# Performance work log

Hardware: AMD Instinct MI355X
Metric: run time of the kernel (lower is better)

The kernel has to match this reference:

```python
import jax, jax.numpy as jnp
import numpy as np

L, B, S, D, H, F, V = 12, 2, 1024, 768, 12, 3072, 50257
DK = D // H
EPS = 1e-6


def _ln(x, a, b):
    # torch: a*(x-mean)/(std+eps)+b with unbiased std (ddof=1)
    m = x.mean(-1, keepdims=True)
    std = jnp.sqrt(((x - m) ** 2).sum(-1, keepdims=True) / (x.shape[-1] - 1))
    return a * (x - m) / (std + EPS) + b


def _pos_encoding(s, d):
    pos = jnp.arange(s, dtype=jnp.float32)[:, None]
    div = jnp.exp(jnp.arange(0, d, 2, dtype=jnp.float32) * (-np.log(10000.0) / d))
    pe = jnp.zeros((s, d), dtype=jnp.float32)
    pe = pe.at[:, 0::2].set(jnp.sin(pos * div))
    pe = pe.at[:, 1::2].set(jnp.cos(pos * div))
    return pe


def setup_inputs() -> dict:
    key = jax.random.key(0)
    ks = jax.random.split(key, 8)
    n = lambda k, sh: 0.02 * jax.random.normal(k, sh, dtype=jnp.float32)
    return dict(
        emb=n(ks[0], (V, D)),
        Wq=n(ks[1], (L, D, D)),
        Wk=n(ks[2], (L, D, D)),
        Wv=n(ks[3], (L, D, D)),
        Wo=n(ks[4], (L, D, D)),
        ln1_a=jnp.ones((L, D), jnp.float32),
        ln1_b=jnp.zeros((L, D), jnp.float32),
        ln2_a=jnp.ones((L, D), jnp.float32),
        ln2_b=jnp.zeros((L, D), jnp.float32),
        W1=n(ks[5], (L, D, F)),
        b1=jnp.zeros((L, F), jnp.float32),
        W2=n(ks[6], (L, F, D)),
        b2=jnp.zeros((L, D), jnp.float32),
        fn_a=jnp.ones((D,), jnp.float32),
        fn_b=jnp.zeros((D,), jnp.float32),
        pb=jnp.zeros((V,), jnp.float32),
        x=jax.random.randint(ks[7], (B, S), 0, V, dtype=jnp.int32),
    )


def reference(emb, Wq, Wk, Wv, Wo, ln1_a, ln1_b, ln2_a, ln2_b, W1, b1, W2, b2, fn_a, fn_b, pb, x):
    b, s = x.shape
    d = emb.shape[1]
    h = emb[x] * jnp.sqrt(jnp.float32(d)) + _pos_encoding(s, d)  # [B,S,D]
    causal = jnp.tril(jnp.ones((s, s), dtype=bool))

    def block(hh, p):
        wq, wk, wv, wo, a1, bb1n, a2, bb2n, w1, fb1, w2, fb2 = p
        xn = _ln(hh, a1, bb1n)
        q = (xn @ wq).reshape(b, s, H, DK)
        k = (xn @ wk).reshape(b, s, H, DK)
        v = (xn @ wv).reshape(b, s, H, DK)
        scores = jnp.einsum('bqhd,bkhd->bhqk', q, k) / jnp.sqrt(jnp.float32(DK))
        scores = jnp.where(causal, scores, -1e9)  # masked_fill_(mask==0, -1e9)
        attn = jax.nn.softmax(scores, axis=-1)
        o = jnp.einsum('bhqk,bkhd->bqhd', attn, v).reshape(b, s, d)
        hh = hh + o @ wo
        xn2 = _ln(hh, a2, bb2n)
        hh = hh + (jax.nn.relu(xn2 @ w1 + fb1) @ w2 + fb2)
        return hh, None

    h, _ = jax.lax.scan(block, h, (Wq, Wk, Wv, Wo, ln1_a, ln1_b, ln2_a, ln2_b, W1, b1, W2, b2))
    h = _ln(h, fn_a, fn_b)
    logits = h @ emb.T + pb  # tied-weight projection
    return logits
```

## Files before the change

### kernel.cpp

```cpp
#include <hip/hip_runtime.h>
#include <math.h>

constexpr int Lc = 12, Bc = 2, Sc = 1024, Dc = 768, Hc = 12, Fc = 3072, Vc = 50257, DKc = 64;
constexpr int Tc = Bc * Sc;
constexpr int QKVN = 3 * Dc;
constexpr int Vpad = 50304;

typedef __attribute__((ext_vector_type(8))) __bf16 bf16x8;
typedef __attribute__((ext_vector_type(8))) unsigned short u16x8;
typedef __attribute__((ext_vector_type(4))) float f32x4;

__device__ __forceinline__ unsigned short f2b(float f) {
  union { float f; unsigned int u; } v; v.f = f;
  unsigned int r = v.u + 0x7FFFu + ((v.u >> 16) & 1u);
  return (unsigned short)(r >> 16);
}
__device__ __forceinline__ float b2f(unsigned short u) {
  return __uint_as_float(((unsigned int)u) << 16);
}

__device__ __forceinline__ void gload16(const void* g, void* l) {
  __builtin_amdgcn_global_load_lds((const __attribute__((address_space(1))) void*)g,
                                   (__attribute__((address_space(3))) void*)l, 16, 0, 0);
}

__device__ __forceinline__ float bred_sum(float v, volatile float* sb) {
#pragma unroll
  for (int o = 32; o; o >>= 1) v += __shfl_down(v, o);
  int w = threadIdx.x >> 6;
  __syncthreads();
  if ((threadIdx.x & 63) == 0) sb[w] = v;
  __syncthreads();
  return sb[0] + sb[1] + sb[2] + sb[3];
}

__global__ __launch_bounds__(256) void embed_kernel(const float* __restrict__ emb,
                                                    const int* __restrict__ x,
                                                    float* __restrict__ h) {
  int t = blockIdx.x;
  int s = t & (Sc - 1);
  int tok = x[t];
  const float scale = 27.712812921102035f;
  for (int d = threadIdx.x; d < Dc; d += 256) {
    int i = d >> 1;
    float div = __expf((float)(2 * i) * (-9.210340371976184f / (float)Dc));
    float ang = (float)s * div;
    float pe = (d & 1) ? cosf(ang) : sinf(ang);
    h[(size_t)t * Dc + d] = emb[(size_t)tok * Dc + d] * scale + pe;
  }
}

__global__ __launch_bounds__(256) void convert_emb_kernel(const float* __restrict__ emb,
                                                          ushort* __restrict__ embT) {
  const size_t total4 = (size_t)Vpad * Dc / 4;
  for (size_t i = (size_t)blockIdx.x * 256 + threadIdx.x; i < total4; i += (size_t)gridDim.x * 256) {
    size_t e = i * 4;
    int row = (int)(e / Dc);
    ushort4 w;
    if (row < Vc) {
      float4 f = *(const float4*)&emb[e];
      w.x = f2b(f.x); w.y = f2b(f.y); w.z = f2b(f.z); w.w = f2b(f.w);
    } else {
      w = make_ushort4(0, 0, 0, 0);
    }
    *(ushort4*)&embT[e] = w;
  }
}

__global__ __launch_bounds__(256) void transpose_layer_kernel(
    const float* __restrict__ Wq, const float* __restrict__ Wk, const float* __restrict__ Wv,
    const float* __restrict__ Wo, const float* __restrict__ W1, const float* __restrict__ W2,
    int l, ushort* __restrict__ WqkvT, ushort* __restrict__ WoT,
    ushort* __restrict__ W1T, ushort* __restrict__ W2T) {
  __shared__ float tile[64][65];
  int bid = blockIdx.x;
  const float* src; ushort* dst; int N, Kd, tt;
  if (bid < 432) {
    int m = bid / 144; tt = bid % 144;
    src = (m == 0 ? Wq : (m == 1 ? Wk : Wv)) + (size_t)l * Dc * Dc;
    N = Dc; Kd = Dc; dst = WqkvT + (size_t)m * Dc * Dc;
  } else if (bid < 576) {
    tt = bid - 432; src = Wo + (size_t)l * Dc * Dc; N = Dc; Kd = Dc; dst = WoT;
  } else if (bid < 1152) {
    tt = bid - 576; src = W1 + (size_t)l * Dc * Fc; N = Fc; Kd = Dc; dst = W1T;
  } else {
    tt = bid - 1152; src = W2 + (size_t)l * Fc * Dc; N = Dc; Kd = Fc; dst = W2T;
  }
  int nt = N / 64;
  int k0 = (tt / nt) * 64, n0 = (tt % nt) * 64;
  int t = threadIdx.x;
  int r0 = t >> 4, c4 = (t & 15) * 4;
#pragma unroll
  for (int rr = 0; rr < 4; ++rr) {
    int r = r0 + rr * 16;
    float4 f = *(const float4*)&src[(size_t)(k0 + r) * N + n0 + c4];
    tile[r][c4] = f.x; tile[r][c4 + 1] = f.y; tile[r][c4 + 2] = f.z; tile[r][c4 + 3] = f.w;
  }
  __syncthreads();
  int i0 = t >> 4, j4 = (t & 15) * 4;
#pragma unroll
  for (int rr = 0; rr < 4; ++rr) {
    int i = i0 + rr * 16;
    ushort4 w;
    w.x = f2b(tile[j4][i]); w.y = f2b(tile[j4 + 1][i]);
    w.z = f2b(tile[j4 + 2][i]); w.w = f2b(tile[j4 + 3][i]);
    *(ushort4*)&dst[(size_t)(n0 + i) * Kd + k0 + j4] = w;
  }
}

__global__ __launch_bounds__(256) void ln_kernel(const float* __restrict__ in,
                                                 const float* __restrict__ ga,
                                                 const float* __restrict__ be,
                                                 ushort* __restrict__ out) {
  __shared__ float sb[4];
  int t = blockIdx.x;
  const float* row = in + (size_t)t * Dc;
  int tid = threadIdx.x;
  float x0 = row[tid], x1 = row[tid + 256], x2 = row[tid + 512];
  float s = bred_sum(x0 + x1 + x2, sb);
  float mean = s * (1.0f / 768.0f);
  float d0 = x0 - mean, d1 = x1 - mean, d2 = x2 - mean;
  float vs = bred_sum(d0 * d0 + d1 * d1 + d2 * d2, sb);
  float inv = 1.0f / (sqrtf(vs * (1.0f / 767.0f)) + 1e-6f);
  ushort* orow = out + (size_t)t * Dc;
  orow[tid] = f2b(ga[tid] * d0 * inv + be[tid]);
  orow[tid + 256] = f2b(ga[tid + 256] * d1 * inv + be[tid + 256]);
  orow[tid + 512] = f2b(ga[tid + 512] * d2 * inv + be[tid + 512]);
}

template <typename OT, int BM, bool BIAS, bool RELU, bool RESID, bool SWAP>
__global__ __launch_bounds__(256) void gemm_bf16(const ushort* __restrict__ A,
                                                 const ushort* __restrict__ Bt,
                                                 const float* __restrict__ bias,
                                                 const float* __restrict__ resid,
                                                 OT* __restrict__ C,
                                                 int M, int N, int K, int ldc) {
  constexpr int MW = BM / 64;
  constexpr int NW = 4 / MW;
  constexpr int WCOLS = 128 / NW;
  constexpr int NJ = WCOLS / 16;
  __shared__ __attribute__((aligned(16))) ushort sm[(BM + 128) * 32];
  ushort* As = sm;
  ushort* Bs = sm + BM * 32;
  const int tid = threadIdx.x;
  const int wid = tid >> 6, lane = tid & 63;
  const int wr = (MW == 2) ? (wid >> 1) : 0;
  const int wc = (MW == 2) ? (wid & 1) : wid;
  const int kg = lane >> 4, fr = lane & 15;
  const int bm = (SWAP ? blockIdx.x : blockIdx.y) * BM;
  const int bn = (SWAP ? blockIdx.y : blockIdx.x) * 128;

  f32x4 acc[4][NJ] = {};

  for (int k0 = 0; k0 < K; k0 += 32) {
    const ushort* Ab = A + (size_t)bm * K + k0;
    const ushort* Bb = Bt + (size_t)bn * K + k0;
#pragma unroll
    for (int it = 0; it < BM / 64; ++it) {
      int c = it * 256 + tid;
      int row = c >> 2, kc = (c & 3) * 8;
      gload16(Ab + (size_t)row * K + kc, &As[(it * 256 + wid * 64) * 8]);
    }
#pragma unroll
    for (int it = 0; it < 2; ++it) {
      int c = it * 256 + tid;
      int row = c >> 2, kc = (c & 3) * 8;
      gload16(Bb + (size_t)row * K + kc, &Bs[(it * 256 + wid * 64) * 8]);
    }
    __syncthreads();

    bf16x8 af[4], bfr[NJ];
#pragma unroll
    for (int i = 0; i < 4; ++i)
      af[i] = *(const bf16x8*)&As[(wr * 64 + i * 16 + fr) * 32 + kg * 8];
#pragma unroll
    for (int j = 0; j < NJ; ++j)
      bfr[j] = *(const bf16x8*)&Bs[(wc * WCOLS + j * 16 + fr) * 32 + kg * 8];
#pragma unroll
    for (int i = 0; i < 4; ++i)
#pragma unroll
      for (int j = 0; j < NJ; ++j)
        acc[i][j] = __builtin_amdgcn_mfma_f32_16x16x32_bf16(af[i], bfr[j], acc[i][j], 0, 0, 0);
    __syncthreads();
  }

  const int r0 = kg * 4;
#pragma unroll
  for (int i = 0; i < 4; ++i) {
    int mbase = bm + wr * 64 + i * 16 + r0;
#pragma unroll
    for (int j = 0; j < NJ; ++j) {
      int n = bn + wc * WCOLS + j * 16 + fr;
      if (n < N) {
        float bv = BIAS ? bias[n] : 0.0f;
#pragma unroll
        for (int r = 0; r < 4; ++r) {
          float v = acc[i][j][r] + bv;
          if (RELU) v = fmaxf(v, 0.0f);
          size_t idx = (size_t)(mbase + r) * ldc + n;
          if (RESID) v += resid[idx];
          if constexpr (sizeof(OT) == 2) C[idx] = (OT)f2b(v);
          else C[idx] = (OT)v;
        }
      }
    }
  }
}

__global__ __launch_bounds__(256) void flash_attn_kernel(const ushort* __restrict__ qkv,
                                                         ushort* __restrict__ o) {
  const int qt = gridDim.x - 1 - blockIdx.x;
  const int hb = blockIdx.y;
  const int hh = hb % Hc, b = hb / Hc;
  const int tid = threadIdx.x;
  const int w = tid >> 6, lane = tid & 63;
  const int g = lane >> 4, c = lane & 15;

  __shared__ __attribute__((aligned(16))) ushort Ks[64 * 64];
  __shared__ __attribute__((aligned(16))) ushort Vt[64 * 64];
  __shared__ __attribute__((aligned(16))) ushort Ps[4][16 * 64];

  const int q0 = qt * 64;
  const int qw = q0 + w * 16;

  bf16x8 aq[2];
  {
    const size_t qrow = (size_t)(b * Sc + qw + c) * QKVN + hh * DKc;
#pragma unroll
    for (int kk = 0; kk < 2; ++kk)
      aq[kk] = *(const bf16x8*)&qkv[qrow + kk * 32 + g * 8];
  }

  float m_r[4], l_r[4];
  f32x4 oa[4] = {};
#pragma unroll
  for (int r = 0; r < 4; ++r) { m_r[r] = -1e30f; l_r[r] = 0.f; }

  const int ntiles = qt + 1;
  for (int t = 0; t < ntiles; ++t) {
    const int kv0 = t * 64;
#pragma unroll
    for (int it = 0; it < 2; ++it) {
      int idx = it * 256 + tid;
      int kv = idx >> 3, ck = idx & 7;
      u16x8 kd = *(const u16x8*)&qkv[(size_t)(b * Sc + kv0 + kv) * QKVN + Dc + hh * DKc + ck * 8];
      *(u16x8*)((char*)Ks + ((kv * 128 + ck * 16) ^ ((kv & 7) << 4))) = kd;
    }
    {
      int kv = tid >> 2;
      int dbase = (tid & 3) * 16;
      const ushort* vrow = &qkv[(size_t)(b * Sc + kv0 + kv) * QKVN + 2 * Dc + hh * DKc + dbase];
      u16x8 v0 = *(const u16x8*)&vrow[0];
      u16x8 v1 = *(const u16x8*)&vrow[8];
#pragma unroll
      for (int dd = 0; dd < 8; ++dd) {
        int d0 = dbase + dd, d1 = dbase + 8 + dd;
        *(ushort*)((char*)Vt + ((d0 * 128 + kv * 2) ^ ((d0 & 7) << 4))) = v0[dd];
        *(ushort*)((char*)Vt + ((d1 * 128 + kv * 2) ^ ((d1 & 7) << 4))) = v1[dd];
      }
    }
    __syncthreads();

    f32x4 sacc[4] = {};
#pragma unroll
    for (int jn = 0; jn < 4; ++jn) {
      int kvl = jn * 16 + c;
#pragma unroll
      for (int kk = 0; kk < 2; ++kk) {
        bf16x8 bk = *(const bf16x8*)((char*)Ks + ((kvl * 128 + kk * 64 + g * 16) ^ ((kvl & 7) << 4)));
        sacc[jn] = __builtin_amdgcn_mfma_f32_16x16x32_bf16(aq[kk], bk, sacc[jn], 0, 0, 0);
      }
    }

    const bool last = (t == ntiles - 1);
    float p[4][4];
#pragma unroll
    for (int jn = 0; jn < 4; ++jn) {
      int kvg = kv0 + jn * 16 + c;
#pragma unroll
      for (int r = 0; r < 4; ++r) {
        float s = sacc[jn][r] * 0.125f;
        if (last && kvg > qw + g * 4 + r) s = -1e30f;
        p[jn][r] = s;
      }
    }
#pragma unroll
    for (int r = 0; r < 4; ++r) {
      float mx = fmaxf(fmaxf(p[0][r], p[1][r]), fmaxf(p[2][r], p[3][r]));
#pragma unroll
      for (int off = 1; off < 16; off <<= 1) mx = fmaxf(mx, __shfl_xor(mx, off));
      float mnew = fmaxf(m_r[r], mx);
      float sf = __expf(m_r[r] - mnew);
      m_r[r] = mnew;
      float rs = 0.f;
#pragma unroll
      for (int jn = 0; jn < 4; ++jn) {
        float e = __expf(p[jn][r] - mnew);
        p[jn][r] = e;
        rs += e;
      }
#pragma unroll
      for (int off = 1; off < 16; off <<= 1) rs += __shfl_xor(rs, off);
      l_r[r] = l_r[r] * sf + rs;
#pragma unroll
      for (int jd = 0; jd < 4; ++jd) oa[jd][r] *= sf;
    }

    {
      ushort* pw = Ps[w];
#pragma unroll
      for (int jn = 0; jn < 4; ++jn)
#pragma unroll
        for (int r = 0; r < 4; ++r) {
          int row = g * 4 + r, col = jn * 16 + c;
          *(ushort*)((char*)pw + ((row * 128 + col * 2) ^ ((row & 7) << 4))) = f2b(p[jn][r]);
        }
      bf16x8 ap[2];
#pragma unroll
      for (int kk = 0; kk < 2; ++kk)
        ap[kk] = *(const bf16x8*)((char*)pw + ((c * 128 + kk * 64 + g * 16) ^ ((c & 7) << 4)));
#pragma unroll
      for (int jd = 0; jd < 4; ++jd) {
        int d = jd * 16 + c;
#pragma unroll
        for (int kk = 0; kk < 2; ++kk) {
          bf16x8 bv = *(const bf16x8*)((char*)Vt + ((d * 128 + kk * 64 + g * 16) ^ ((d & 7) << 4)));
          oa[jd] = __builtin_amdgcn_mfma_f32_16x16x32_bf16(ap[kk], bv, oa[jd], 0, 0, 0);
        }
      }
    }
    __syncthreads();
  }

#pragma unroll
  for (int r = 0; r < 4; ++r) {
    int q = qw + g * 4 + r;
    float inv = 1.0f / l_r[r];
    size_t base = (size_t)(b * Sc + q) * Dc + hh * DKc;
#pragma unroll
    for (int jd = 0; jd < 4; ++jd)
      o[base + jd * 16 + c] = f2b(oa[jd][r] * inv);
  }
}

extern "C" void kernel_launch(void* const* d_in, const int* in_sizes, int n_in,
                              void* d_out, int out_size, void* d_ws, size_t ws_size,
                              hipStream_t stream) {
  const float* emb  = (const float*)d_in[0];
  const float* Wq   = (const float*)d_in[1];
  const float* Wk   = (const float*)d_in[2];
  const float* Wv   = (const float*)d_in[3];
  const float* Wo   = (const float*)d_in[4];
  const float* ln1a = (const float*)d_in[5];
  const float* ln1b = (const float*)d_in[6];
  const float* ln2a = (const float*)d_in[7];
  const float* ln2b = (const float*)d_in[8];
  const float* W1   = (const float*)d_in[9];
  const float* b1   = (const float*)d_in[10];
  const float* W2   = (const float*)d_in[11];
  const float* b2   = (const float*)d_in[12];
  const float* fna  = (const float*)d_in[13];
  const float* fnb  = (const float*)d_in[14];
  const float* pb   = (const float*)d_in[15];
  const int*   x    = (const int*)d_in[16];
  float* out = (float*)d_out;

  float* h = (float*)d_ws;
  ushort* xn    = (ushort*)(h + (size_t)Tc * Dc);
  ushort* qkv   = xn + (size_t)Tc * Dc;
  ushort* ao    = qkv + (size_t)Tc * QKVN;
  ushort* f1    = ao + (size_t)Tc * Dc;
  ushort* embT  = f1 + (size_t)Tc * Fc;
  ushort* WqkvT = embT + (size_t)Vpad * Dc;
  ushort* WoT   = WqkvT + (size_t)QKVN * Dc;
  ushort* W1T   = WoT + (size_t)Dc * Dc;
  ushort* W2T   = W1T + (size_t)Fc * Dc;

  embed_kernel<<<Tc, 256, 0, stream>>>(emb, x, h);
  convert_emb_kernel<<<2048, 256, 0, stream>>>(emb, embT);

  dim3 gQKV(QKVN / 128, Tc / 128);
  dim3 gD64(Dc / 128, Tc / 64);
  dim3 gF(Fc / 128, Tc / 128);
  dim3 gA(Sc / 64, Bc * Hc);
  for (int l = 0; l < Lc; ++l) {
    transpose_layer_kernel<<<1728, 256, 0, stream>>>(Wq, Wk, Wv, Wo, W1, W2, l,
                                                     WqkvT, WoT, W1T, W2T);
    ln_kernel<<<Tc, 256, 0, stream>>>(h, ln1a + l * Dc, ln1b + l * Dc, xn);
    gemm_bf16<ushort, 128, false, false, false, false><<<gQKV, 256, 0, stream>>>(
        xn, WqkvT, nullptr, nullptr, qkv, Tc, QKVN, Dc, QKVN);
    flash_attn_kernel<<<gA, 256, 0, stream>>>(qkv, ao);
    gemm_bf16<float, 64, false, false, true, false><<<gD64, 256, 0, stream>>>(
        ao, WoT, nullptr, h, h, Tc, Dc, Dc, Dc);
    ln_kernel<<<Tc, 256, 0, stream>>>(h, ln2a + l * Dc, ln2b + l * Dc, xn);
    gemm_bf16<ushort, 128, true, true, false, false><<<gF, 256, 0, stream>>>(
        xn, W1T, b1 + (size_t)l * Fc, nullptr, f1, Tc, Fc, Dc, Fc);
    gemm_bf16<float, 64, true, false, true, false><<<gD64, 256, 0, stream>>>(
        f1, W2T, b2 + (size_t)l * Dc, h, h, Tc, Dc, Fc, Dc);
  }
  ln_kernel<<<Tc, 256, 0, stream>>>(h, fna, fnb, xn);
  dim3 gL(Tc / 128, Vpad / 128);
  gemm_bf16<float, 128, true, false, false, true><<<gL, 256, 0, stream>>>(
      xn, embT, pb, nullptr, out, Tc, Vc, Dc, Vc);
}
```

Baseline: 3.010 ms.

## Deepen GEMM K-tile, add V pre-transpose, widen attention KV tiles

The GEMM K-step doubles from 32 to 64, so there are half as many barrier-separated iterations and more MFMA work per LDS fill. A separate kernel writes V transposed per head, which lets the attention kernel load K and V straight into swizzled LDS with global_load_lds instead of scattered scalar stores. Attention now handles 128 KV positions per tile and uses exp2 with a log2e-folded scale. In exchange there is one extra kernel launch and round trip through memory per layer, more LDS per block (which may lower occupancy), and partial masking on the last tile when the query tile index is even.

```diff
diff --git a/kernel.cpp b/kernel.cpp
--- a/kernel.cpp
+++ b/kernel.cpp
@@ -108,6 +108,31 @@
   }
 }
 
+__global__ __launch_bounds__(256) void vtrans_kernel(const ushort* __restrict__ qkv,
+                                                     ushort* __restrict__ vT) {
+  __shared__ ushort tl[64][72];
+  const int st = blockIdx.x, hb = blockIdx.y;
+  const int hh = hb % Hc, b = hb / Hc;
+  const int t0 = st * 64;
+  const int tid = threadIdx.x;
+  {
+    int r = tid >> 2, cg = (tid & 3) * 16;
+    const ushort* src = qkv + (size_t)(b * Sc + t0 + r) * QKVN + 2 * Dc + hh * DKc + cg;
+    *(u16x8*)&tl[r][cg] = *(const u16x8*)&src[0];
+    *(u16x8*)&tl[r][cg + 8] = *(const u16x8*)&src[8];
+  }
+  __syncthreads();
+  {
+    int d = tid >> 2, tg = (tid & 3) * 16;
+    u16x8 o0, o1;
+#pragma unroll
+    for (int j = 0; j < 8; ++j) { o0[j] = tl[tg + j][d]; o1[j] = tl[tg + 8 + j][d]; }
+    ushort* dst = vT + (size_t)hb * DKc * Sc + (size_t)d * Sc + t0 + tg;
+    *(u16x8*)&dst[0] = o0;
+    *(u16x8*)&dst[8] = o1;
+  }
+}
+
 __global__ __launch_bounds__(256) void ln_kernel(const float* __restrict__ in,
                                                  const float* __restrict__ ga,
                                                  const float* __restrict__ be,
@@ -139,9 +164,9 @@
   constexpr int NW = 4 / MW;
   constexpr int WCOLS = 128 / NW;
   constexpr int NJ = WCOLS / 16;
-  __shared__ __attribute__((aligned(16))) ushort sm[(BM + 128) * 32];
+  __shared__ __attribute__((aligned(16))) ushort sm[(BM + 128) * 64];
   ushort* As = sm;
-  ushort* Bs = sm + BM * 32;
+  ushort* Bs = sm + BM * 64;
   const int tid = threadIdx.x;
   const int wid = tid >> 6, lane = tid & 63;
   const int wr = (MW == 2) ? (wid >> 1) : 0;
@@ -152,35 +177,38 @@
 
   f32x4 acc[4][NJ] = {};
 
-  for (int k0 = 0; k0 < K; k0 += 32) {
+  for (int k0 = 0; k0 < K; k0 += 64) {
     const ushort* Ab = A + (size_t)bm * K + k0;
     const ushort* Bb = Bt + (size_t)bn * K + k0;
 #pragma unroll
-    for (int it = 0; it < BM / 64; ++it) {
-      int c = it * 256 + tid;
-      int row = c >> 2, kc = (c & 3) * 8;
+    for (int it = 0; it < BM / 32; ++it) {
+      int s = it * 256 + tid;
+      int row = s >> 3, kc = (s & 7) * 8;
       gload16(Ab + (size_t)row * K + kc, &As[(it * 256 + wid * 64) * 8]);
     }
 #pragma unroll
-    for (int it = 0; it < 2; ++it) {
-      int c = it * 256 + tid;
-      int row = c >> 2, kc = (c & 3) * 8;
+    for (int it = 0; it < 4; ++it) {
+      int s = it * 256 + tid;
+      int row = s >> 3, kc = (s & 7) * 8;
       gload16(Bb + (size_t)row * K + kc, &Bs[(it * 256 + wid * 64) * 8]);
     }
     __syncthreads();
 
-    bf16x8 af[4], bfr[NJ];
-#pragma unroll
-    for (int i = 0; i < 4; ++i)
-      af[i] = *(const bf16x8*)&As[(wr * 64 + i * 16 + fr) * 32 + kg * 8];
-#pragma unroll
-    for (int j = 0; j < NJ; ++j)
-      bfr[j] = *(const bf16x8*)&Bs[(wc * WCOLS + j * 16 + fr) * 32 + kg * 8];
-#pragma unroll
-    for (int i = 0; i < 4; ++i)
+#pragma unroll
+    for (int hk = 0; hk < 2; ++hk) {
+      bf16x8 af[4], bfr[NJ];
+#pragma unroll
+      for (int i = 0; i < 4; ++i)
+        af[i] = *(const bf16x8*)&As[(wr * 64 + i * 16 + fr) * 64 + hk * 32 + kg * 8];
 #pragma unroll
       for (int j = 0; j < NJ; ++j)
-        acc[i][j] = __builtin_amdgcn_mfma_f32_16x16x32_bf16(af[i], bfr[j], acc[i][j], 0, 0, 0);
+        bfr[j] = *(const bf16x8*)&Bs[(wc * WCOLS + j * 16 + fr) * 64 + hk * 32 + kg * 8];
+#pragma unroll
+      for (int i = 0; i < 4; ++i)
+#pragma unroll
+        for (int j = 0; j < NJ; ++j)
+          acc[i][j] = __builtin_amdgcn_mfma_f32_16x16x32_bf16(af[i], bfr[j], acc[i][j], 0, 0, 0);
+    }
     __syncthreads();
   }
 
@@ -208,6 +236,7 @@
 }
 
 __global__ __launch_bounds__(256) void flash_attn_kernel(const ushort* __restrict__ qkv,
+                                                         const ushort* __restrict__ vT,
                                                          ushort* __restrict__ o) {
   const int qt = gridDim.x - 1 - blockIdx.x;
   const int hb = blockIdx.y;
@@ -216,9 +245,9 @@
   const int w = tid >> 6, lane = tid & 63;
   const int g = lane >> 4, c = lane & 15;
 
-  __shared__ __attribute__((aligned(16))) ushort Ks[64 * 64];
-  __shared__ __attribute__((aligned(16))) ushort Vt[64 * 64];
-  __shared__ __attribute__((aligned(16))) ushort Ps[4][16 * 64];
+  __shared__ __attribute__((aligned(16))) ushort Ks[128 * 64];
+  __shared__ __attribute__((aligned(16))) ushort Vs[64 * 128];
+  __shared__ __attribute__((aligned(16))) ushort Ps[4][16 * 128];
 
   const int q0 = qt * 64;
   const int qw = q0 + w * 16;
@@ -236,34 +265,34 @@
 #pragma unroll
   for (int r = 0; r < 4; ++r) { m_r[r] = -1e30f; l_r[r] = 0.f; }
 
-  const int ntiles = qt + 1;
-  for (int t = 0; t < ntiles; ++t) {
-    const int kv0 = t * 64;
-#pragma unroll
-    for (int it = 0; it < 2; ++it) {
-      int idx = it * 256 + tid;
-      int kv = idx >> 3, ck = idx & 7;
-      u16x8 kd = *(const u16x8*)&qkv[(size_t)(b * Sc + kv0 + kv) * QKVN + Dc + hh * DKc + ck * 8];
-      *(u16x8*)((char*)Ks + ((kv * 128 + ck * 16) ^ ((kv & 7) << 4))) = kd;
-    }
-    {
-      int kv = tid >> 2;
-      int dbase = (tid & 3) * 16;
-      const ushort* vrow = &qkv[(size_t)(b * Sc + kv0 + kv) * QKVN + 2 * Dc + hh * DKc + dbase];
-      u16x8 v0 = *(const u16x8*)&vrow[0];
-      u16x8 v1 = *(const u16x8*)&vrow[8];
-#pragma unroll
-      for (int dd = 0; dd < 8; ++dd) {
-        int d0 = dbase + dd, d1 = dbase + 8 + dd;
-        *(ushort*)((char*)Vt + ((d0 * 128 + kv * 2) ^ ((d0 & 7) << 4))) = v0[dd];
-        *(ushort*)((char*)Vt + ((d1 * 128 + kv * 2) ^ ((d1 & 7) << 4))) = v1[dd];
-      }
+  const ushort* kbase = qkv + (size_t)b * Sc * QKVN + Dc + hh * DKc;
+  const ushort* vbase = vT + (size_t)hb * DKc * Sc;
+  const float kS = 0.18033688011112042f;
+
+  const int KT = (qt + 2) >> 1;
+  for (int t = 0; t < KT; ++t) {
+    const int kv0 = t * 128;
+#pragma unroll
+    for (int it = 0; it < 4; ++it) {
+      int s = it * 256 + tid;
+      int kv = s >> 3;
+      int dkb = ((s & 7) * 16) ^ ((kv & 7) << 4);
+      gload16(kbase + (size_t)(kv0 + kv) * QKVN + (dkb >> 1),
+              (char*)Ks + (it * 256 + w * 64) * 16);
+    }
+#pragma unroll
+    for (int it = 0; it < 4; ++it) {
+      int s = it * 256 + tid;
+      int d = s >> 4;
+      int kvb = ((s & 15) * 16) ^ ((d & 7) << 4);
+      gload16(vbase + (size_t)d * Sc + kv0 + (kvb >> 1),
+              (char*)Vs + (it * 256 + w * 64) * 16);
     }
     __syncthreads();
 
-    f32x4 sacc[4] = {};
-#pragma unroll
-    for (int jn = 0; jn < 4; ++jn) {
+    f32x4 sacc[8] = {};
+#pragma unroll
+    for (int jn = 0; jn < 8; ++jn) {
       int kvl = jn * 16 + c;
 #pragma unroll
       for (int kk = 0; kk < 2; ++kk) {
@@ -272,31 +301,35 @@
       }
     }
 
-    const bool last = (t == ntiles - 1);
-    float p[4][4];
-#pragma unroll
-    for (int jn = 0; jn < 4; ++jn) {
-      int kvg = kv0 + jn * 16 + c;
-#pragma unroll
-      for (int r = 0; r < 4; ++r) {
-        float s = sacc[jn][r] * 0.125f;
-        if (last && kvg > qw + g * 4 + r) s = -1e30f;
-        p[jn][r] = s;
+#pragma unroll
+    for (int jn = 0; jn < 8; ++jn)
+#pragma unroll
+      for (int r = 0; r < 4; ++r) sacc[jn][r] *= kS;
+    if (t == KT - 1) {
+#pragma unroll
+      for (int jn = 0; jn < 8; ++jn) {
+        int kvg = kv0 + jn * 16 + c;
+#pragma unroll
+        for (int r = 0; r < 4; ++r)
+          if (kvg > qw + g * 4 + r) sacc[jn][r] = -1e30f;
       }
     }
+
 #pragma unroll
     for (int r = 0; r < 4; ++r) {
-      float mx = fmaxf(fmaxf(p[0][r], p[1][r]), fmaxf(p[2][r], p[3][r]));
+      float mx = sacc[0][r];
+#pragma unroll
+      for (int jn = 1; jn < 8; ++jn) mx = fmaxf(mx, sacc[jn][r]);
 #pragma unroll
       for (int off = 1; off < 16; off <<= 1) mx = fmaxf(mx, __shfl_xor(mx, off));
       float mnew = fmaxf(m_r[r], mx);
-      float sf = __expf(m_r[r] - mnew);
+      float sf = exp2f(m_r[r] - mnew);
       m_r[r] = mnew;
       float rs = 0.f;
 #pragma unroll
-      for (int jn = 0; jn < 4; ++jn) {
-        float e = __expf(p[jn][r] - mnew);
-        p[jn][r] = e;
+      for (int jn = 0; jn < 8; ++jn) {
+        float e = exp2f(sacc[jn][r] - mnew);
+        sacc[jn][r] = e;
         rs += e;
       }
 #pragma unroll
@@ -309,22 +342,22 @@
     {
       ushort* pw = Ps[w];
 #pragma unroll
-      for (int jn = 0; jn < 4; ++jn)
+      for (int jn = 0; jn < 8; ++jn)
 #pragma unroll
         for (int r = 0; r < 4; ++r) {
           int row = g * 4 + r, col = jn * 16 + c;
-          *(ushort*)((char*)pw + ((row * 128 + col * 2) ^ ((row & 7) << 4))) = f2b(p[jn][r]);
+          *(ushort*)((char*)pw + ((row * 256 + col * 2) ^ ((row & 7) << 4))) = f2b(sacc[jn][r]);
         }
-      bf16x8 ap[2];
-#pragma unroll
-      for (int kk = 0; kk < 2; ++kk)
-        ap[kk] = *(const bf16x8*)((char*)pw + ((c * 128 + kk * 64 + g * 16) ^ ((c & 7) << 4)));
+      bf16x8 ap[4];
+#pragma unroll
+      for (int kk = 0; kk < 4; ++kk)
+        ap[kk] = *(const bf16x8*)((char*)pw + ((c * 256 + kk * 64 + g * 16) ^ ((c & 7) << 4)));
 #pragma unroll
       for (int jd = 0; jd < 4; ++jd) {
         int d = jd * 16 + c;
 #pragma unroll
-        for (int kk = 0; kk < 2; ++kk) {
-          bf16x8 bv = *(const bf16x8*)((char*)Vt + ((d * 128 + kk * 64 + g * 16) ^ ((d & 7) << 4)));
+        for (int kk = 0; kk < 4; ++kk) {
+          bf16x8 bv = *(const bf16x8*)((char*)Vs + ((d * 256 + kk * 64 + g * 16) ^ ((d & 7) << 4)));
           oa[jd] = __builtin_amdgcn_mfma_f32_16x16x32_bf16(ap[kk], bv, oa[jd], 0, 0, 0);
         }
       }
@@ -370,7 +403,8 @@
   ushort* qkv   = xn + (size_t)Tc * Dc;
   ushort* ao    = qkv + (size_t)Tc * QKVN;
   ushort* f1    = ao + (size_t)Tc * Dc;
-  ushort* embT  = f1 + (size_t)Tc * Fc;
+  ushort* vT    = f1 + (size_t)Tc * Fc;
+  ushort* embT  = vT + (size_t)Bc * Hc * DKc * Sc;
   ushort* WqkvT = embT + (size_t)Vpad * Dc;
   ushort* WoT   = WqkvT + (size_t)QKVN * Dc;
   ushort* W1T   = WoT + (size_t)Dc * Dc;
@@ -383,13 +417,15 @@
   dim3 gD64(Dc / 128, Tc / 64);
   dim3 gF(Fc / 128, Tc / 128);
   dim3 gA(Sc / 64, Bc * Hc);
+  dim3 gV(Sc / 64, Bc * Hc);
   for (int l = 0; l < Lc; ++l) {
     transpose_layer_kernel<<<1728, 256, 0, stream>>>(Wq, Wk, Wv, Wo, W1, W2, l,
                                                      WqkvT, WoT, W1T, W2T);
     ln_kernel<<<Tc, 256, 0, stream>>>(h, ln1a + l * Dc, ln1b + l * Dc, xn);
     gemm_bf16<ushort, 128, false, false, false, false><<<gQKV, 256, 0, stream>>>(
         xn, WqkvT, nullptr, nullptr, qkv, Tc, QKVN, Dc, QKVN);
-    flash_attn_kernel<<<gA, 256, 0, stream>>>(qkv, ao);
+    vtrans_kernel<<<gV, 256, 0, stream>>>(qkv, vT);
+    flash_attn_kernel<<<gA, 256, 0, stream>>>(qkv, vT, ao);
     gemm_bf16<float, 64, false, false, true, false><<<gD64, 256, 0, stream>>>(
         ao, WoT, nullptr, h, h, Tc, Dc, Dc, Dc);
     ln_kernel<<<Tc, 256, 0, stream>>>(h, ln2a + l * Dc, ln2b + l * Dc, xn);
```

Measured after the change: 2.998 ms. No clear change (-0.4%).
